# Kernel optimization log

Hardware: AMD Instinct MI355X
Metric: run time of the kernel (lower is better)

The kernel has to match this reference:

```python
import jax, jax.numpy as jnp
import numpy as np

N_TOKENS = 8192
NQ = 6
NL = 2


def ry_mat(theta):
    # theta: scalar or (B,) -> (2,2) or (B,2,2) complex RY matrix
    c = jnp.cos(theta / 2)
    s = jnp.sin(theta / 2)
    return jnp.stack([jnp.stack([c, -s], -1), jnp.stack([s, c], -1)], -2).astype(jnp.complex64)


def apply_1q(state, gate, q, nq):
    # state: (B, 2**nq); gate: (2,2) shared or (B,2,2) per-batch
    B = state.shape[0]
    st = state.reshape(B, 2 ** q, 2, -1)
    if gate.ndim == 3:
        st = jnp.einsum('bij,bajc->baic', gate, st)
    else:
        st = jnp.einsum('ij,bajc->baic', gate, st)
    return st.reshape(B, -1)


def apply_rz(state, theta, q, nq):
    # diagonal RZ: multiply phases, no matmul needed
    B = state.shape[0]
    st = state.reshape(B, 2 ** q, 2, -1)
    ph = jnp.stack([jnp.exp(-0.5j * theta), jnp.exp(0.5j * theta)]).astype(jnp.complex64)
    return (st * ph[None, None, :, None]).reshape(B, -1)


def apply_cnot(state, c, t, nq):
    B = state.shape[0]
    st = state.reshape((B,) + (2,) * nq)
    s0 = jnp.take(st, 0, axis=1 + c)
    s1 = jnp.take(st, 1, axis=1 + c)
    ta = 1 + t - (1 if t > c else 0)  # target axis after removing control axis
    s1 = jnp.flip(s1, axis=ta)
    st = jnp.stack([s0, s1], axis=1 + c)
    return st.reshape(B, -1)


def prepare_states(x, params, nl, nq):
    # x: (B, nq) angles; params: (nl, nq, 2). Returns (B, 2**nq) complex statevectors.
    B = x.shape[0]
    state = jnp.zeros((B, 2 ** nq), jnp.complex64).at[:, 0].set(1.0)
    for q in range(nq):  # RY angle embedding
        state = apply_1q(state, ry_mat(x[:, q]), q, nq)
    for l in range(nl):  # PQC layers: RY, RZ rotations + CNOT ring
        for q in range(nq):
            state = apply_1q(state, ry_mat(params[l, q, 0]), q, nq)
            state = apply_rz(state, params[l, q, 1], q, nq)
        for q in range(nq):
            state = apply_cnot(state, q, (q + 1) % nq, nq)
    return state


def setup_inputs() -> dict:
    key = jax.random.key(0)
    k1, k2, k3, k4 = jax.random.split(key, 4)
    return {
        'x_tokens': jax.random.normal(k1, (N_TOKENS, NQ), dtype=jnp.float32),
        'params_q': 0.1 * jax.random.normal(k2, (NL, NQ, 2), dtype=jnp.float32),
        'params_k': 0.1 * jax.random.normal(k3, (NL, NQ, 2), dtype=jnp.float32),
        'params_v': 0.1 * jax.random.normal(k4, (NL, NQ, 2), dtype=jnp.float32),
    }


def reference(x_tokens, params_q, params_k, params_v):
    nq = x_tokens.shape[1]
    nl = params_q.shape[0]
    sq = prepare_states(x_tokens, params_q, nl, nq)  # (N, 2**nq)
    sk = prepare_states(x_tokens, params_k, nl, nq)
    ov = jnp.einsum('id,jd->ij', sq, jnp.conj(sk))  # pairwise overlaps (N, N)
    logits = jnp.real(ov * jnp.conj(ov))            # swap-test fidelity |<q|k>|^2
    attn = jax.nn.softmax(logits, axis=-1)
    sv = prepare_states(x_tokens, params_v, nl, nq)
    probs = jnp.real(sv * jnp.conj(sv))             # (N, 2**nq)
    idx = jnp.arange(2 ** nq)
    bits = (idx[None, :] >> (nq - 1 - jnp.arange(nq))[:, None]) & 1  # (nq, 2**nq)
    signs = (1.0 - 2.0 * bits).astype(probs.dtype)
    V = probs @ signs.T                              # <Z_q> per qubit -> (N, nq)
    return attn @ V
```

## Files before the change

### kernel.cpp

```cpp
#include <hip/hip_runtime.h>
#include <hip/hip_bf16.h>
#include <hip/hip_fp16.h>

#define NT 8192
#define NQB 6
#define NL 2
#define JSPLIT 16
#define JSLICE (NT / JSPLIT)
#define CHUNK 32
#define NCHUNK (JSLICE / CHUNK)
#define IPW 32
#define WPB 4
#define IPB (IPW * WPB)
#define NBI (NT / IPB)
#define WSTRIDE 40

typedef _Float16 f16x8 __attribute__((ext_vector_type(8)));
typedef float f32x4 __attribute__((ext_vector_type(4)));

static __device__ __forceinline__ unsigned int pack_h2(float a, float b) {
  unsigned short lo = __builtin_bit_cast(unsigned short, (_Float16)a);
  unsigned short hi = __builtin_bit_cast(unsigned short, (_Float16)b);
  return (unsigned int)lo | ((unsigned int)hi << 16);
}

static __device__ __forceinline__ unsigned int pkrtz(float a, float b) {
  return __builtin_bit_cast(unsigned int, __builtin_amdgcn_cvt_pkrtz(a, b));
}

static __device__ __forceinline__ int cnot_src(int p, int q) {
  const int mc = 1 << (5 - q);
  const int mt = 1 << (5 - ((q + 1) % NQB));
  return (p & mc) ? (p ^ mt) : p;
}

#define GLOAD_LDS16(g, l)                                      \
  __builtin_amdgcn_global_load_lds(                            \
      (const __attribute__((address_space(1))) void*)(g),      \
      (__attribute__((address_space(3))) void*)(l), 16, 0, 0)

__global__ __launch_bounds__(256) void prep_kernel(
    const float* __restrict__ x, const float* __restrict__ pq,
    const float* __restrict__ pk, const float* __restrict__ pv,
    unsigned int* __restrict__ Are, unsigned int* __restrict__ Bk,
    unsigned short* __restrict__ Vt)
{
  const int wid  = blockIdx.x * 4 + (threadIdx.x >> 6);
  const int lane = threadIdx.x & 63;
  const int set  = wid >> 13;
  const int tok  = wid & (NT - 1);
  const float* pp = (set == 0) ? pq : ((set == 1) ? pk : pv);

  int m = lane;
#pragma unroll
  for (int q = 5; q >= 0; --q) m = cnot_src(m, q);
  int inv = lane;
#pragma unroll
  for (int q = 0; q < 6; ++q) inv = cnot_src(inv, q);

  float a = 0.f;
  if (lane < 6)                    a = 0.5f * x[tok * NQB + lane];
  else if (lane >= 8 && lane < 14) a = 0.5f * pp[(lane - 8) * 2];
  else if (lane >= 16 && lane < 22) a = 0.5f * pp[12 + (lane - 16) * 2];
  float sa, ca;
  __sincosf(a, &sa, &ca);

  float R = 1.f;
#pragma unroll
  for (int q = 0; q < 6; ++q) {
    const float tqs = __shfl(sa, q, 64),     tqc = __shfl(ca, q, 64);
    const float prs = __shfl(sa, 8 + q, 64), prc = __shfl(ca, 8 + q, 64);
    const float s = tqs * prc + tqc * prs;
    const float c = tqc * prc - tqs * prs;
    R *= ((m >> (5 - q)) & 1) ? s : c;
  }
  float phi0 = 0.f;
#pragma unroll
  for (int q = 0; q < 6; ++q) {
    const float bh = 0.5f * pp[q * 2 + 1];
    phi0 += ((m >> (5 - q)) & 1) ? bh : -bh;
  }
  float s0, c0;
  __sincosf(phi0, &s0, &c0);
  float re = R * c0, im = R * s0;

#pragma unroll
  for (int q = 0; q < 6; ++q) {
    const int mask = 1 << (5 - q);
    const float rcs = __shfl(sa, 16 + q, 64), rcc = __shfl(ca, 16 + q, 64);
    const float pre = __shfl_xor(re, mask, 64);
    const float pim = __shfl_xor(im, mask, 64);
    const float se = (lane & mask) ? rcs : -rcs;
    re = fmaf(se, pre, rcc * re);
    im = fmaf(se, pim, rcc * im);
  }
  float phi1 = 0.f;
#pragma unroll
  for (int q = 0; q < 6; ++q) {
    const float bh = 0.5f * pp[12 + q * 2 + 1];
    phi1 += ((lane >> (5 - q)) & 1) ? bh : -bh;
  }
  float s1, c1;
  __sincosf(phi1, &s1, &c1);
  const float fre = re * c1 - im * s1;
  const float fim = re * s1 + im * c1;

  if (set == 0) {
    Are[tok * 64 + inv] = pack_h2(fre, fim);
  } else if (set == 1) {
    const int sidx = ((((inv >> 2) ^ (tok & 15)) << 2) | (inv & 3));
    Bk[tok * 64 + sidx] = pack_h2(fre, fim);
  } else {
    const float prob = fre * fre + fim * fim;
    float vq[NQB];
#pragma unroll
    for (int q = 0; q < NQB; ++q) {
      float v = (inv & (1 << (5 - q))) ? -prob : prob;
#pragma unroll
      for (int off = 1; off < 64; off <<= 1) v += __shfl_xor(v, off, 64);
      vq[q] = v;
    }
    if (lane < 16) {
      const int q = lane & 7;
      float sel = vq[0];
      if (q == 1) sel = vq[1];
      if (q == 2) sel = vq[2];
      if (q == 3) sel = vq[3];
      if (q == 4) sel = vq[4];
      if (q == 5) sel = vq[5];
      if (q == 6) sel = 1.0f;
      if (q == 7) sel = 0.0f;
      float outv;
      if (lane < 8) {
        outv = sel;
      } else {
        const float hi = (float)(_Float16)sel;
        outv = (q < 6) ? (sel - hi) : 0.0f;
      }
      Vt[lane * NT + tok] = __builtin_bit_cast(unsigned short, (_Float16)outv);
    }
  }
}

__global__ __launch_bounds__(256, 2) void attn_kernel(
    const uint4* __restrict__ Are, const uint4* __restrict__ Bk,
    const unsigned short* __restrict__ Vt, float* __restrict__ part)
{
  __shared__ uint4 kbuf[3][CHUNK * 16];
  __shared__ __align__(16) unsigned short wbuf[WPB][2][16][WSTRIDE];

  const int tid  = threadIdx.x;
  const int lane = tid & 63;
  const int wave = tid >> 6;
  const int col  = lane & 15;
  const int quad = lane >> 4;

  const int ib = blockIdx.x & (NBI - 1);
  const int js = blockIdx.x >> 6;
  const int ibase = ib * IPB + wave * IPW;
  const int jbase0 = js * JSLICE;

  f16x8 qRe[2][4], qIm[2][4];
#pragma unroll
  for (int rt = 0; rt < 2; ++rt) {
    const uint4* pr = Are + (ibase + rt * 16 + col) * 16 + quad;
#pragma unroll
    for (int s = 0; s < 4; ++s) {
      const uint4 u = pr[s * 4];
      uint4 w;
      w.x = ((u.x << 16) | (u.x >> 16)) ^ 0x80000000u;
      w.y = ((u.y << 16) | (u.y >> 16)) ^ 0x80000000u;
      w.z = ((u.z << 16) | (u.z >> 16)) ^ 0x80000000u;
      w.w = ((u.w << 16) | (u.w >> 16)) ^ 0x80000000u;
      qRe[rt][s] = __builtin_bit_cast(f16x8, u);
      qIm[rt][s] = __builtin_bit_cast(f16x8, w);
    }
  }

  int koff[4];
#pragma unroll
  for (int s = 0; s < 4; ++s) koff[s] = (((s * 4 + quad) ^ col) << 4);

  f32x4 acc[2] = {{0.f, 0.f, 0.f, 0.f}, {0.f, 0.f, 0.f, 0.f}};

  const uint4* sbase = Bk + (size_t)jbase0 * 16 + (size_t)(wave * 2) * 64 + lane;
  auto stage = [&](int buf, int c) {
    const uint4* src = sbase + (size_t)c * (CHUNK * 16);
    GLOAD_LDS16(src,      &kbuf[buf][(wave * 2 + 0) * 64]);
    GLOAD_LDS16(src + 64, &kbuf[buf][(wave * 2 + 1) * 64]);
  };

  stage(0, 0);
  __builtin_amdgcn_sched_barrier(0);
  stage(1, 1);
  asm volatile("s_waitcnt vmcnt(2)" ::: "memory");
  __builtin_amdgcn_s_barrier();
  asm volatile("" ::: "memory");

  const unsigned short* vtp = Vt + (size_t)col * NT + jbase0 + quad * 8;

  int cur = 0;
#pragma unroll 1
  for (int c = 0; c < NCHUNK; ++c) {
    if (c + 2 < NCHUNK) {
      int nb = cur + 2; if (nb >= 3) nb -= 3;
      stage(nb, c + 2);
    }
    const f16x8 vb = *(const f16x8*)(vtp + c * CHUNK);

#pragma unroll
    for (int ct = 0; ct < 2; ++ct) {
      const char* kb = (const char*)kbuf[cur] + (ct * 16 + col) * 256;
      f16x8 bfr[4];
#pragma unroll
      for (int s = 0; s < 4; ++s) bfr[s] = *(const f16x8*)(kb + koff[s]);
#pragma unroll
      for (int rt = 0; rt < 2; ++rt) {
        f32x4 aR = {0.f, 0.f, 0.f, 0.f};
        f32x4 aI = {0.f, 0.f, 0.f, 0.f};
        __builtin_amdgcn_s_setprio(1);
#pragma unroll
        for (int s = 0; s < 4; ++s) {
          aR = __builtin_amdgcn_mfma_f32_16x16x32_f16(bfr[s], qRe[rt][s], aR, 0, 0, 0);
          aI = __builtin_amdgcn_mfma_f32_16x16x32_f16(bfr[s], qIm[rt][s], aI, 0, 0, 0);
        }
        __builtin_amdgcn_s_setprio(0);
        const float w0 = __expf(aR[0] * aR[0] + aI[0] * aI[0]);
        const float w1 = __expf(aR[1] * aR[1] + aI[1] * aI[1]);
        const float w2 = __expf(aR[2] * aR[2] + aI[2] * aI[2]);
        const float w3 = __expf(aR[3] * aR[3] + aI[3] * aI[3]);
        *(uint2*)&wbuf[wave][rt][col][ct * 16 + quad * 4] =
            make_uint2(pkrtz(w0, w1), pkrtz(w2, w3));
      }
    }
    {
      const f16x8 wA0 = *(const f16x8*)&wbuf[wave][0][col][quad * 8];
      const f16x8 wA1 = *(const f16x8*)&wbuf[wave][1][col][quad * 8];
      acc[0] = __builtin_amdgcn_mfma_f32_16x16x32_f16(wA0, vb, acc[0], 0, 0, 0);
      acc[1] = __builtin_amdgcn_mfma_f32_16x16x32_f16(wA1, vb, acc[1], 0, 0, 0);
    }

    if (c + 1 < NCHUNK) {
      if (c + 2 < NCHUNK) asm volatile("s_waitcnt vmcnt(2)" ::: "memory");
      else                asm volatile("s_waitcnt vmcnt(0)" ::: "memory");
      __builtin_amdgcn_s_barrier();
      asm volatile("" ::: "memory");
    }
    cur = (cur + 1 == 3) ? 0 : cur + 1;
  }

#pragma unroll
  for (int rt = 0; rt < 2; ++rt) {
    float res[4];
#pragma unroll
    for (int r = 0; r < 4; ++r) res[r] = acc[rt][r] + __shfl_xor(acc[rt][r], 8, 64);
    if (col < 8) {
      float* p = part + ((size_t)(js * NT + ibase + rt * 16 + quad * 4)) * 8 + col;
#pragma unroll
      for (int r = 0; r < 4; ++r) p[r * 8] = res[r];
    }
  }
}

__global__ __launch_bounds__(256) void combine_kernel(
    const float* __restrict__ part, float* __restrict__ out)
{
  const int row = blockIdx.x * 256 + threadIdx.x;
  float acc[7] = {0.f, 0.f, 0.f, 0.f, 0.f, 0.f, 0.f};
#pragma unroll
  for (int js = 0; js < JSPLIT; ++js) {
    const float* p = part + ((size_t)(js * NT + row)) * 8;
#pragma unroll
    for (int q = 0; q < 7; ++q) acc[q] += p[q];
  }
  const float inv = 1.0f / acc[6];
#pragma unroll
  for (int q = 0; q < 6; ++q)
    out[row * 6 + q] = acc[q] * inv;
}

extern "C" void kernel_launch(void* const* d_in, const int* in_sizes, int n_in,
                              void* d_out, int out_size, void* d_ws, size_t ws_size,
                              hipStream_t stream) {
  const float* x  = (const float*)d_in[0];
  const float* pq = (const float*)d_in[1];
  const float* pk = (const float*)d_in[2];
  const float* pv = (const float*)d_in[3];
  char* ws = (char*)d_ws;
  unsigned int*   Are = (unsigned int*)(ws);
  unsigned int*   Bk  = (unsigned int*)(ws + (size_t)(2u << 20));
  unsigned short* Vt  = (unsigned short*)(ws + (size_t)(4u << 20));
  float*          prt = (float*)(ws + (size_t)(4u << 20) + (size_t)(256u << 10));

  prep_kernel<<<(NT * 3) / 4, 256, 0, stream>>>(x, pq, pk, pv, Are, Bk, Vt);
  attn_kernel<<<NBI * JSPLIT, 256, 0, stream>>>((const uint4*)Are, (const uint4*)Bk,
                                                Vt, prt);
  combine_kernel<<<NT / 256, 256, 0, stream>>>(prt, (float*)d_out);
}
```

Measured before the change: 143.6 us.

## Load K fragments directly from global into registers, dropping LDS staging

Replaces the triple-buffered global-to-LDS staging of K tiles (with block-wide barriers) by per-wave direct global loads into register fragments, double-buffered in registers across the two 16-column subtiles. The XOR swizzle on the K layout in the prep kernel is removed since LDS bank conflicts no longer apply. This removes the per-chunk s_barrier and the LDS reads. In exchange each of the four waves independently fetches the same K data from L2/L1, so global traffic rises and register pressure grows.

```diff
diff --git a/kernel.cpp b/kernel.cpp
--- a/kernel.cpp
+++ b/kernel.cpp
@@ -34,11 +34,6 @@
   return (p & mc) ? (p ^ mt) : p;
 }
 
-#define GLOAD_LDS16(g, l)                                      \
-  __builtin_amdgcn_global_load_lds(                            \
-      (const __attribute__((address_space(1))) void*)(g),      \
-      (__attribute__((address_space(3))) void*)(l), 16, 0, 0)
-
 __global__ __launch_bounds__(256) void prep_kernel(
     const float* __restrict__ x, const float* __restrict__ pq,
     const float* __restrict__ pk, const float* __restrict__ pv,
@@ -108,8 +103,7 @@
   if (set == 0) {
     Are[tok * 64 + inv] = pack_h2(fre, fim);
   } else if (set == 1) {
-    const int sidx = ((((inv >> 2) ^ (tok & 15)) << 2) | (inv & 3));
-    Bk[tok * 64 + sidx] = pack_h2(fre, fim);
+    Bk[tok * 64 + inv] = pack_h2(fre, fim);
   } else {
     const float prob = fre * fre + fim * fim;
     float vq[NQB];
@@ -146,7 +140,6 @@
     const uint4* __restrict__ Are, const uint4* __restrict__ Bk,
     const unsigned short* __restrict__ Vt, float* __restrict__ part)
 {
-  __shared__ uint4 kbuf[3][CHUNK * 16];
   __shared__ __align__(16) unsigned short wbuf[WPB][2][16][WSTRIDE];
 
   const int tid  = threadIdx.x;
@@ -177,76 +170,53 @@
     }
   }
 
-  int koff[4];
-#pragma unroll
-  for (int s = 0; s < 4; ++s) koff[s] = (((s * 4 + quad) ^ col) << 4);
-
   f32x4 acc[2] = {{0.f, 0.f, 0.f, 0.f}, {0.f, 0.f, 0.f, 0.f}};
 
-  const uint4* sbase = Bk + (size_t)jbase0 * 16 + (size_t)(wave * 2) * 64 + lane;
-  auto stage = [&](int buf, int c) {
-    const uint4* src = sbase + (size_t)c * (CHUNK * 16);
-    GLOAD_LDS16(src,      &kbuf[buf][(wave * 2 + 0) * 64]);
-    GLOAD_LDS16(src + 64, &kbuf[buf][(wave * 2 + 1) * 64]);
+  const uint4* kbase = Bk + (size_t)(jbase0 + col) * 16 + quad;
+  auto loadK = [&](f16x8 (&kf)[4], int g) {
+    const uint4* a = kbase + g * 256;
+#pragma unroll
+    for (int s = 0; s < 4; ++s) kf[s] = __builtin_bit_cast(f16x8, a[s * 4]);
   };
 
-  stage(0, 0);
-  __builtin_amdgcn_sched_barrier(0);
-  stage(1, 1);
-  asm volatile("s_waitcnt vmcnt(2)" ::: "memory");
-  __builtin_amdgcn_s_barrier();
-  asm volatile("" ::: "memory");
+  auto qk = [&](const f16x8 (&kf)[4], int ct) {
+#pragma unroll
+    for (int rt = 0; rt < 2; ++rt) {
+      f32x4 aR = {0.f, 0.f, 0.f, 0.f};
+      f32x4 aI = {0.f, 0.f, 0.f, 0.f};
+      __builtin_amdgcn_s_setprio(1);
+#pragma unroll
+      for (int s = 0; s < 4; ++s) {
+        aR = __builtin_amdgcn_mfma_f32_16x16x32_f16(kf[s], qRe[rt][s], aR, 0, 0, 0);
+        aI = __builtin_amdgcn_mfma_f32_16x16x32_f16(kf[s], qIm[rt][s], aI, 0, 0, 0);
+      }
+      __builtin_amdgcn_s_setprio(0);
+      const float w0 = __expf(aR[0] * aR[0] + aI[0] * aI[0]);
+      const float w1 = __expf(aR[1] * aR[1] + aI[1] * aI[1]);
+      const float w2 = __expf(aR[2] * aR[2] + aI[2] * aI[2]);
+      const float w3 = __expf(aR[3] * aR[3] + aI[3] * aI[3]);
+      *(uint2*)&wbuf[wave][rt][col][ct * 16 + quad * 4] =
+          make_uint2(pkrtz(w0, w1), pkrtz(w2, w3));
+    }
+  };
 
   const unsigned short* vtp = Vt + (size_t)col * NT + jbase0 + quad * 8;
 
-  int cur = 0;
+  f16x8 kA[4], kB[4];
+  loadK(kA, 0);
+  loadK(kB, 1);
+
 #pragma unroll 1
   for (int c = 0; c < NCHUNK; ++c) {
-    if (c + 2 < NCHUNK) {
-      int nb = cur + 2; if (nb >= 3) nb -= 3;
-      stage(nb, c + 2);
-    }
     const f16x8 vb = *(const f16x8*)(vtp + c * CHUNK);
-
-#pragma unroll
-    for (int ct = 0; ct < 2; ++ct) {
-      const char* kb = (const char*)kbuf[cur] + (ct * 16 + col) * 256;
-      f16x8 bfr[4];
-#pragma unroll
-      for (int s = 0; s < 4; ++s) bfr[s] = *(const f16x8*)(kb + koff[s]);
-#pragma unroll
-      for (int rt = 0; rt < 2; ++rt) {
-        f32x4 aR = {0.f, 0.f, 0.f, 0.f};
-        f32x4 aI = {0.f, 0.f, 0.f, 0.f};
-        __builtin_amdgcn_s_setprio(1);
-#pragma unroll
-        for (int s = 0; s < 4; ++s) {
-          aR = __builtin_amdgcn_mfma_f32_16x16x32_f16(bfr[s], qRe[rt][s], aR, 0, 0, 0);
-          aI = __builtin_amdgcn_mfma_f32_16x16x32_f16(bfr[s], qIm[rt][s], aI, 0, 0, 0);
-        }
-        __builtin_amdgcn_s_setprio(0);
-        const float w0 = __expf(aR[0] * aR[0] + aI[0] * aI[0]);
-        const float w1 = __expf(aR[1] * aR[1] + aI[1] * aI[1]);
-        const float w2 = __expf(aR[2] * aR[2] + aI[2] * aI[2]);
-        const float w3 = __expf(aR[3] * aR[3] + aI[3] * aI[3]);
-        *(uint2*)&wbuf[wave][rt][col][ct * 16 + quad * 4] =
-            make_uint2(pkrtz(w0, w1), pkrtz(w2, w3));
-      }
-    }
-    {
-      const f16x8 wA0 = *(const f16x8*)&wbuf[wave][0][col][quad * 8];
-      const f16x8 wA1 = *(const f16x8*)&wbuf[wave][1][col][quad * 8];
-      acc[0] = __builtin_amdgcn_mfma_f32_16x16x32_f16(wA0, vb, acc[0], 0, 0, 0);
-      acc[1] = __builtin_amdgcn_mfma_f32_16x16x32_f16(wA1, vb, acc[1], 0, 0, 0);
-    }
-
-    if (c + 1 < NCHUNK) {
-      if (c + 2 < NCHUNK) asm volatile("s_waitcnt vmcnt(2)" ::: "memory");
-      else                asm volatile("s_waitcnt vmcnt(0)" ::: "memory");
-      __builtin_amdgcn_s_barrier();
-      asm volatile("" ::: "memory");
-    }
-    cur = (cur + 1 == 3) ? 0 : cur + 1;
+    qk(kA, 0);
+    if (c + 1 < NCHUNK) loadK(kA, 2 * c + 2);
+    qk(kB, 1);
+    if (c + 1 < NCHUNK) loadK(kB, 2 * c + 3);
+    const f16x8 wA0 = *(const f16x8*)&wbuf[wave][0][col][quad * 8];
+    const f16x8 wA1 = *(const f16x8*)&wbuf[wave][1][col][quad * 8];
+    acc[0] = __builtin_amdgcn_mfma_f32_16x16x32_f16(wA0, vb, acc[0], 0, 0, 0);
+    acc[1] = __builtin_amdgcn_mfma_f32_16x16x32_f16(wA1, vb, acc[1], 0, 0, 0);
   }
 
 #pragma unroll
```

Result: slower. 177.0 us (+23.3%).

## Feed exp weights straight from MFMA accumulators into PV MFMA, skipping LDS

Applied to the files above, without the earlier changes.

The softmax weights produced in the QK MFMA accumulator layout are now packed to fp16 and used directly as the A operand of a 16x16x16 MFMA against V. This removes the per-wave LDS staging buffer and its store/load round trip. The key buffering drops from triple to double buffering with full vmcnt(0) waits, and the j-split doubles to 32 so more blocks run. The combine kernel reads partial sums as float4 pairs. The trade-offs are a doubled partial-sum buffer, a shallower prefetch pipeline and narrower-K MFMAs.

```diff
diff --git a/kernel.cpp b/kernel.cpp
--- a/kernel.cpp
+++ b/kernel.cpp
@@ -5,7 +5,7 @@
 #define NT 8192
 #define NQB 6
 #define NL 2
-#define JSPLIT 16
+#define JSPLIT 32
 #define JSLICE (NT / JSPLIT)
 #define CHUNK 32
 #define NCHUNK (JSLICE / CHUNK)
@@ -13,9 +13,9 @@
 #define WPB 4
 #define IPB (IPW * WPB)
 #define NBI (NT / IPB)
-#define WSTRIDE 40
 
 typedef _Float16 f16x8 __attribute__((ext_vector_type(8)));
+typedef _Float16 f16x4 __attribute__((ext_vector_type(4)));
 typedef float f32x4 __attribute__((ext_vector_type(4)));
 
 static __device__ __forceinline__ unsigned int pack_h2(float a, float b) {
@@ -146,8 +146,7 @@
     const uint4* __restrict__ Are, const uint4* __restrict__ Bk,
     const unsigned short* __restrict__ Vt, float* __restrict__ part)
 {
-  __shared__ uint4 kbuf[3][CHUNK * 16];
-  __shared__ __align__(16) unsigned short wbuf[WPB][2][16][WSTRIDE];
+  __shared__ uint4 kbuf[2][CHUNK * 16];
 
   const int tid  = threadIdx.x;
   const int lane = tid & 63;
@@ -191,22 +190,16 @@
   };
 
   stage(0, 0);
-  __builtin_amdgcn_sched_barrier(0);
-  stage(1, 1);
-  asm volatile("s_waitcnt vmcnt(2)" ::: "memory");
+  asm volatile("s_waitcnt vmcnt(0)" ::: "memory");
   __builtin_amdgcn_s_barrier();
   asm volatile("" ::: "memory");
 
-  const unsigned short* vtp = Vt + (size_t)col * NT + jbase0 + quad * 8;
-
-  int cur = 0;
+  const unsigned short* vtp = Vt + (size_t)col * NT + jbase0 + quad * 4;
+
 #pragma unroll 1
   for (int c = 0; c < NCHUNK; ++c) {
-    if (c + 2 < NCHUNK) {
-      int nb = cur + 2; if (nb >= 3) nb -= 3;
-      stage(nb, c + 2);
-    }
-    const f16x8 vb = *(const f16x8*)(vtp + c * CHUNK);
+    const int cur = c & 1;
+    if (c + 1 < NCHUNK) stage(cur ^ 1, c + 1);
 
 #pragma unroll
     for (int ct = 0; ct < 2; ++ct) {
@@ -214,6 +207,7 @@
       f16x8 bfr[4];
 #pragma unroll
       for (int s = 0; s < 4; ++s) bfr[s] = *(const f16x8*)(kb + koff[s]);
+      const f16x4 vb = *(const f16x4*)(vtp + c * CHUNK + ct * 16);
 #pragma unroll
       for (int rt = 0; rt < 2; ++rt) {
         f32x4 aR = {0.f, 0.f, 0.f, 0.f};
@@ -229,24 +223,17 @@
         const float w1 = __expf(aR[1] * aR[1] + aI[1] * aI[1]);
         const float w2 = __expf(aR[2] * aR[2] + aI[2] * aI[2]);
         const float w3 = __expf(aR[3] * aR[3] + aI[3] * aI[3]);
-        *(uint2*)&wbuf[wave][rt][col][ct * 16 + quad * 4] =
-            make_uint2(pkrtz(w0, w1), pkrtz(w2, w3));
+        uint2 wp = make_uint2(pkrtz(w0, w1), pkrtz(w2, w3));
+        const f16x4 wa = __builtin_bit_cast(f16x4, wp);
+        acc[rt] = __builtin_amdgcn_mfma_f32_16x16x16f16(wa, vb, acc[rt], 0, 0, 0);
       }
     }
-    {
-      const f16x8 wA0 = *(const f16x8*)&wbuf[wave][0][col][quad * 8];
-      const f16x8 wA1 = *(const f16x8*)&wbuf[wave][1][col][quad * 8];
-      acc[0] = __builtin_amdgcn_mfma_f32_16x16x32_f16(wA0, vb, acc[0], 0, 0, 0);
-      acc[1] = __builtin_amdgcn_mfma_f32_16x16x32_f16(wA1, vb, acc[1], 0, 0, 0);
-    }
 
     if (c + 1 < NCHUNK) {
-      if (c + 2 < NCHUNK) asm volatile("s_waitcnt vmcnt(2)" ::: "memory");
-      else                asm volatile("s_waitcnt vmcnt(0)" ::: "memory");
+      asm volatile("s_waitcnt vmcnt(0)" ::: "memory");
       __builtin_amdgcn_s_barrier();
       asm volatile("" ::: "memory");
     }
-    cur = (cur + 1 == 3) ? 0 : cur + 1;
   }
 
 #pragma unroll
@@ -269,9 +256,11 @@
   float acc[7] = {0.f, 0.f, 0.f, 0.f, 0.f, 0.f, 0.f};
 #pragma unroll
   for (int js = 0; js < JSPLIT; ++js) {
-    const float* p = part + ((size_t)(js * NT + row)) * 8;
-#pragma unroll
-    for (int q = 0; q < 7; ++q) acc[q] += p[q];
+    const float4* p4 = (const float4*)(part + ((size_t)(js * NT + row)) * 8);
+    const float4 a = p4[0];
+    const float4 b = p4[1];
+    acc[0] += a.x; acc[1] += a.y; acc[2] += a.z; acc[3] += a.w;
+    acc[4] += b.x; acc[5] += b.y; acc[6] += b.z;
   }
   const float inv = 1.0f / acc[6];
 #pragma unroll
```

Measured after the change: 146.0 us. Within noise of the previous version (+1.7%).
